# Kernel tuning notes

Measured on AMD Instinct MI355X. Metric: run time of the kernel, lower is better.

The kernel has to match this reference:

```python
import jax, jax.numpy as jnp
import numpy as np

N_NODES = 100000
N_EDGES = 800000
NODE_DIM = 64
EDGE_DIM = 64
GEO_DIM = 8
GEO_OUT = 32
COND_DIM = 512
N_GRAPHS = 64
JOIN_DIM = EDGE_DIM + GEO_OUT  # 96


def setup_inputs() -> dict:
    key = jax.random.key(0)
    ks = jax.random.split(key, 10)
    return {
        "node_feats": jax.random.normal(ks[0], (N_NODES, NODE_DIM), jnp.float32),
        "edge_index": jax.random.randint(ks[1], (2, N_EDGES), 0, N_NODES, jnp.int64),
        "e_geo": jax.random.normal(ks[2], (N_EDGES, GEO_DIM), jnp.float32),
        "cond": jax.random.normal(ks[3], (N_GRAPHS, COND_DIM), jnp.float32),
        "edge_batch_ids": jax.random.randint(ks[4], (N_EDGES,), 0, N_GRAPHS, jnp.int64),
        "Wn": jax.random.normal(ks[5], (NODE_DIM, EDGE_DIM), jnp.float32) / np.sqrt(NODE_DIM),
        "bn": jnp.zeros((EDGE_DIM,), jnp.float32),
        "Wg": jax.random.normal(ks[6], (GEO_DIM, GEO_OUT), jnp.float32) / np.sqrt(GEO_DIM),
        "bg": jnp.zeros((GEO_OUT,), jnp.float32),
        "Wc": jax.random.normal(ks[7], (COND_DIM, 2 * EDGE_DIM), jnp.float32) / np.sqrt(COND_DIM),
        "bc": jnp.zeros((2 * EDGE_DIM,), jnp.float32),
        "Wx": jax.random.normal(ks[8], (JOIN_DIM, EDGE_DIM), jnp.float32) / np.sqrt(JOIN_DIM),
    }


def reference(node_feats, edge_index, e_geo, cond, edge_batch_ids,
              Wn, bn, Wg, bg, Wc, bc, Wx):
    # n_proj: project node features  [N, node_dim] -> [N, edge_dim]
    n_proj = node_feats @ Wn + bn
    # combine_node_attr 'mul': gather to edge endpoints and multiply  [E, edge_dim]
    src = n_proj[edge_index[0]]
    dst = n_proj[edge_index[1]]
    n_join = src * dst
    # e_geo_linear: [E, geo_dim] -> [E, geo_out]
    eg = e_geo @ Wg + bg
    # join features [E, edge_dim + geo_out]
    join = jnp.concatenate([n_join, eg], axis=-1)
    # FilmFusion: cond_proj -> gamma/beta per graph, gather to edges
    gb = cond @ Wc + bc                      # [B, 2*edge_dim]
    gamma, beta = jnp.split(gb, 2, axis=-1)
    gamma = gamma + 1.0
    gamma_e = gamma[edge_batch_ids]          # [E, edge_dim]
    beta_e = beta[edge_batch_ids]
    # x_linear (bias=False), FiLM modulation, relu
    x = join @ Wx
    return jax.nn.relu(x * gamma_e + beta_e)
```

## Files before the change

### kernel.cpp

```cpp
#include <hip/hip_runtime.h>

#define N_NODES   100000
#define N_EDGES   800000
#define NODE_DIM  64
#define EDGE_DIM  64
#define GEO_DIM   8
#define GEO_OUT   32
#define COND_DIM  512
#define N_GRAPHS  64

#define PREP_BLOCKS   65
#define NPROJ_BLOCKS  3125
#define EDGE_BLOCKS   3125

typedef float          f32x4 __attribute__((ext_vector_type(4)));
typedef unsigned       u32x4 __attribute__((ext_vector_type(4)));
typedef unsigned short u16x8 __attribute__((ext_vector_type(8)));
typedef _Float16       f16x8 __attribute__((ext_vector_type(8)));
typedef _Float16       f16x2 __attribute__((ext_vector_type(2)));

__device__ __forceinline__ unsigned short f2h(float f) {
    _Float16 h = (_Float16)f;
    union { _Float16 h; unsigned short u; } cv;
    cv.h = h;
    return cv.u;
}
__device__ __forceinline__ f16x2 cvt2h(float lo, float hi) {
    f16x2 r;
    r[0] = (_Float16)lo;
    r[1] = (_Float16)hi;
    return r;
}

__global__ __launch_bounds__(256) void pre_kernel(
        const float* __restrict__ cond, const float* __restrict__ Wc,
        const float* __restrict__ bc,   const float* __restrict__ Wg,
        const float* __restrict__ bg,   const float* __restrict__ Wx,
        const float* __restrict__ nf,   const float* __restrict__ Wn,
        const float* __restrict__ bn,
        unsigned* __restrict__ gbpack, unsigned short* __restrict__ Bfrag,
        unsigned short* __restrict__ nprojh) {
    int t = threadIdx.x;
    int g = blockIdx.x;
    if (g < N_GRAPHS) {
        __shared__ float condl[COND_DIM];
        __shared__ float gbl[128];
        for (int i = t; i < COND_DIM; i += 256) condl[i] = cond[g * COND_DIM + i];
        __syncthreads();
        if (t < 128) {
            float acc = bc[t];
            #pragma unroll 8
            for (int k = 0; k < COND_DIM; ++k) acc += condl[k] * Wc[k * 128 + t];
            gbl[t] = acc;
        }
        __syncthreads();
        if (t < 64) {
            float gam = gbl[t] + 1.0f;
            float bet = gbl[64 + t];
            float cv = 0.0f;
            #pragma unroll
            for (int i = 0; i < GEO_OUT; ++i) cv += bg[i] * Wx[(64 + i) * 64 + t];
            union { unsigned u; _Float16 h[2]; } pk;
            pk.h[0] = (_Float16)gam;
            pk.h[1] = (_Float16)(bet + cv * gam);
            gbpack[g * 64 + (((t >> 2) ^ (g & 15)) << 2) + (t & 3)] = pk.u;
        }
    } else if (g == N_GRAPHS) {
        for (int idx = t; idx < 6144; idx += 256) {
            int j    = idx & 7;
            int lane = (idx >> 3) & 63;
            int ct   = idx >> 9;
            int c    = ct >> 2, tt = ct & 3;
            int k = c * 32 + ((lane >> 4) & 3) * 8 + j;
            int n = tt * 16 + (lane & 15);
            float val;
            if (k < 64) {
                val = Wx[k * 64 + n];
            } else if (k < 72) {
                float s = 0.f;
                #pragma unroll
                for (int i = 0; i < GEO_OUT; ++i)
                    s += Wg[(k - 64) * GEO_OUT + i] * Wx[(64 + i) * 64 + n];
                val = s;
            } else {
                val = 0.f;
            }
            Bfrag[idx] = f2h(val);
        }
    } else {
        int lane = t & 63;
        int wid    = ((g - PREP_BLOCKS) * 256 + t) >> 6;
        const int nwaves = (NPROJ_BLOCKS * 256) >> 6;
        float wcol[64];
        #pragma unroll
        for (int k = 0; k < 64; ++k) wcol[k] = Wn[k * 64 + lane];
        float bnl = bn[lane];
        for (int node = wid; node < N_NODES; node += 2 * nwaves) {
            int nu0 = __builtin_amdgcn_readfirstlane(node);
            int nu1 = __builtin_amdgcn_readfirstlane(node + nwaves);
            const float* row0 = nf + (size_t)nu0 * 64;
            const float* row1 = nf + (size_t)nu1 * 64;
            float a0 = 0.f, a1 = 0.f, a2 = 0.f, a3 = bnl;
            float c0 = 0.f, c1 = 0.f, c2 = 0.f, c3 = bnl;
            #pragma unroll
            for (int k = 0; k < 64; k += 4) {
                a0 = fmaf(row0[k    ], wcol[k    ], a0);
                a1 = fmaf(row0[k + 1], wcol[k + 1], a1);
                a2 = fmaf(row0[k + 2], wcol[k + 2], a2);
                a3 = fmaf(row0[k + 3], wcol[k + 3], a3);
                c0 = fmaf(row1[k    ], wcol[k    ], c0);
                c1 = fmaf(row1[k + 1], wcol[k + 1], c1);
                c2 = fmaf(row1[k + 2], wcol[k + 2], c2);
                c3 = fmaf(row1[k + 3], wcol[k + 3], c3);
            }
            nprojh[(size_t)nu0 * 64 + lane] = f2h((a0 + a1) + (a2 + a3));
            nprojh[(size_t)nu1 * 64 + lane] = f2h((c0 + c1) + (c2 + c3));
        }
    }
}

__global__ __launch_bounds__(256, 4) void edge_kernel(
        const unsigned short* __restrict__ nprojh,
        const int*   __restrict__ eidx,
        const float* __restrict__ egeo,
        const int*   __restrict__ ebatch,
        const unsigned short* __restrict__ Bfrag,
        const unsigned* __restrict__ gbpack,
        float* __restrict__ out) {
    int lane = threadIdx.x & 63;
    int q  = lane >> 4;
    int mm = lane & 15;
    int wv = threadIdx.x >> 6;

    __shared__ unsigned short Bl[6144];
    __shared__ unsigned GBl[4096];
    __shared__ float ldsT[4][16 * 64];
    float* tileb = ldsT[wv];

    for (int i = threadIdx.x; i < 768; i += 256)
        ((f32x4*)Bl)[i] = ((const f32x4*)Bfrag)[i];
    for (int i = threadIdx.x; i < 4096; i += 256)
        GBl[i] = gbpack[i];
    __syncthreads();

    const int wbase = mm * 64 + q * 4;
    const int rbase = (lane >> 4) * 64 +
                      (((((lane >> 2) & 3) + (lane >> 4)) & 3) << 4) +
                      (lane & 3) * 4;

    int wid = (blockIdx.x * blockDim.x + threadIdx.x) >> 6;
    const int nwaves = (EDGE_BLOCKS * 256) >> 6;
    const int t0 = wid;

    union HU { u16x8 v; f16x2 h[4]; unsigned u[4]; f16x8 f; };

    HU   sA0, sA1, dA0, dA1;  f32x4 gA0 = {0,0,0,0}, gA1 = {0,0,0,0};
    HU   sB0, sB1, dB0, dB1;  f32x4 gB0 = {0,0,0,0}, gB1 = {0,0,0,0};
    int  bqA[4], bqB[4];
    int  siA, diA, bqiA[4];
    int  siB, diB, bqiB[4];

#define LOAD_IDX(sI, dI, bqI, tl)                                              \
    {                                                                          \
        int e0n = (tl) * 16;                                                   \
        sI = __builtin_nontemporal_load(eidx + e0n + mm);                      \
        dI = __builtin_nontemporal_load(eidx + N_EDGES + e0n + mm);            \
        _Pragma("unroll")                                                      \
        for (int c = 0; c < 4; ++c)                                            \
            bqI[c] = __builtin_nontemporal_load(ebatch + e0n + c * 4 + q);     \
    }

#define GATHER(S0, S1, D0, D1, G0, G1, sI, dI, tl)                             \
    {                                                                          \
        const u16x8* ps = (const u16x8*)(nprojh + (size_t)(sI) * 64 + q * 8);  \
        const u16x8* pd = (const u16x8*)(nprojh + (size_t)(dI) * 64 + q * 8);  \
        S0.v = ps[0]; S1.v = ps[4];                                            \
        D0.v = pd[0]; D1.v = pd[4];                                            \
        if (q == 0) {                                                          \
            int e0n = (tl) * 16;                                               \
            G0 = __builtin_nontemporal_load((const f32x4*)(egeo + (size_t)(e0n + mm) * 8));     \
            G1 = __builtin_nontemporal_load((const f32x4*)(egeo + (size_t)(e0n + mm) * 8 + 4)); \
        }                                                                      \
    }

    {
        int si0, di0, si1, di1;
        LOAD_IDX(si0, di0, bqA, t0);
        LOAD_IDX(si1, di1, bqB, t0 + nwaves);
        LOAD_IDX(siA, diA, bqiA, t0 + 2 * nwaves);
        LOAD_IDX(siB, diB, bqiB, t0 + 3 * nwaves);
        GATHER(sA0, sA1, dA0, dA1, gA0, gA1, si0, di0, t0);
        GATHER(sB0, sB1, dB0, dB1, gB0, gB1, si1, di1, t0 + nwaves);
    }

#define BODY(S0, S1, D0, D1, G0, G1, BQ, tl, PREF, sI, dI, bqI)                \
    {                                                                          \
        int e0 = (tl) * 16;                                                    \
        HU A0, A1, A2;                                                         \
        _Pragma("unroll")                                                      \
        for (int j = 0; j < 4; ++j) {                                          \
            A0.h[j] = S0.h[j] * D0.h[j];                     \
            A1.h[j] = S1.h[j] * D1.h[j];                                       \
            A2.u[j] = 0u;                                                      \
        }                                                                      \
        if (q == 0) {                         \
            A2.h[0] = cvt2h(G0[0], G0[1]);                                     \
            A2.h[1] = cvt2h(G0[2], G0[3]);                                     \
            A2.h[2] = cvt2h(G1[0], G1[1]);                                     \
            A2.h[3] = cvt2h(G1[2], G1[3]);                                     \
        }                                                                      \
        if (PREF)                                  \
            GATHER(S0, S1, D0, D1, G0, G1, sI, dI, (tl) + 2 * nwaves);         \
               \
        f32x4 acc[4];                                                          \
        _Pragma("unroll")                                                      \
        for (int t = 0; t < 4; ++t) {                                          \
            f32x4 c = {0.f, 0.f, 0.f, 0.f};                                    \
            c = __builtin_amdgcn_mfma_f32_16x16x32_f16(                        \
                    *(const f16x8*)(Bl + ((0 * 4 + t) * 64 + lane) * 8), A0.f, c, 0, 0, 0); \
            c = __builtin_amdgcn_mfma_f32_16x16x32_f16(                        \
                    *(const f16x8*)(Bl + ((1 * 4 + t) * 64 + lane) * 8), A1.f, c, 0, 0, 0); \
            c = __builtin_amdgcn_mfma_f32_16x16x32_f16(                        \
                    *(const f16x8*)(Bl + ((2 * 4 + t) * 64 + lane) * 8), A2.f, c, 0, 0, 0); \
            acc[t] = c;                                                        \
        }                                                                      \
        \
        _Pragma("unroll")                                                      \
        for (int t = 0; t < 4; ++t)                                            \
            *(f32x4*)&tileb[wbase + (((t + mm) & 3) << 4)] = acc[t];           \
        asm volatile("s_waitcnt lgkmcnt(0)" ::: "memory");      \
        _Pragma("unroll")                                                      \
        for (int c2 = 0; c2 < 4; ++c2) {                                       \
            int b = BQ[c2];                                                    \
            f32x4 v = *(const f32x4*)&tileb[rbase + c2 * 256];                 \
            u32x4 gb = *(const u32x4*)&GBl[b * 64 + ((mm ^ (b & 15)) << 2)];   \
            f32x4 r;                                                           \
            _Pragma("unroll")                                                  \
            for (int i = 0; i < 4; ++i) {                                      \
                union { unsigned u; _Float16 h[2]; } cv;                       \
                cv.u = gb[i];                                                  \
                float x = fmaf(v[i], (float)cv.h[0], (float)cv.h[1]);          \
                r[i] = x > 0.f ? x : 0.f;                                      \
            }                                                                  \
            __builtin_nontemporal_store(r,                                     \
                (f32x4*)(out + (size_t)e0 * 64 + c2 * 256 + lane * 4));        \
        }                                                                      \
        if (PREF) {                                                            \
            _Pragma("unroll")                                                  \
            for (int c2 = 0; c2 < 4; ++c2) BQ[c2] = bqI[c2];                   \
        }                                                                      \
    }

    BODY(sA0, sA1, dA0, dA1, gA0, gA1, bqA, t0,              true,  siA, diA, bqiA);
    BODY(sB0, sB1, dB0, dB1, gB0, gB1, bqB, t0 + nwaves,     true,  siB, diB, bqiB);
    BODY(sA0, sA1, dA0, dA1, gA0, gA1, bqA, t0 + 2 * nwaves, false, siA, diA, bqiA);
    BODY(sB0, sB1, dB0, dB1, gB0, gB1, bqB, t0 + 3 * nwaves, false, siB, diB, bqiB);

#undef BODY
#undef GATHER
#undef LOAD_IDX
}

extern "C" void kernel_launch(void* const* d_in, const int* in_sizes, int n_in,
                              void* d_out, int out_size, void* d_ws, size_t ws_size,
                              hipStream_t stream) {
    const float* node_feats = (const float*)d_in[0];
    const int*   edge_index = (const int*)  d_in[1];
    const float* e_geo      = (const float*)d_in[2];
    const float* cond       = (const float*)d_in[3];
    const int*   ebatch     = (const int*)  d_in[4];
    const float* Wn         = (const float*)d_in[5];
    const float* bn         = (const float*)d_in[6];
    const float* Wg         = (const float*)d_in[7];
    const float* bg         = (const float*)d_in[8];
    const float* Wc         = (const float*)d_in[9];
    const float* bc         = (const float*)d_in[10];
    const float* Wx         = (const float*)d_in[11];
    float* out = (float*)d_out;

    char* ws = (char*)d_ws;
    unsigned*       gbpack = (unsigned*)(ws);
    unsigned short* Bfrag  = (unsigned short*)(ws + 16384);
    unsigned short* nprojh = (unsigned short*)(ws + 32768);

    hipLaunchKernelGGL(pre_kernel, dim3(PREP_BLOCKS + NPROJ_BLOCKS), dim3(256), 0, stream,
                       cond, Wc, bc, Wg, bg, Wx, node_feats, Wn, bn,
                       gbpack, Bfrag, nprojh);
    hipLaunchKernelGGL(edge_kernel, dim3(EDGE_BLOCKS), dim3(256), 0, stream,
                       nprojh, edge_index, e_geo, ebatch, Bfrag, gbpack, out);
}
```

Before: 335.0 us.

## Shrink edge grid and process ten tiles per wave with rolling index prefetch

Cuts the edge kernel grid from 3125 to 1250 blocks. Each wave now handles ten 16-edge tiles instead of four. The fixed-depth index preload is replaced by a rolling pipeline: each body issues the index loads for the tile four steps ahead and the gather for the tile two steps ahead. This spreads the per-block LDS setup (weight fragments and gamma/beta table) over more work and keeps memory requests in flight across iterations. In exchange there is less parallelism at launch, more live registers, and a longer serial chain per wave.

```diff
diff --git a/kernel.cpp b/kernel.cpp
--- a/kernel.cpp
+++ b/kernel.cpp
@@ -11,7 +11,7 @@
 
 #define PREP_BLOCKS   65
 #define NPROJ_BLOCKS  3125
-#define EDGE_BLOCKS   3125
+#define EDGE_BLOCKS   1250
 
 typedef float          f32x4 __attribute__((ext_vector_type(4)));
 typedef unsigned       u32x4 __attribute__((ext_vector_type(4)));
@@ -156,9 +156,9 @@
 
     HU   sA0, sA1, dA0, dA1;  f32x4 gA0 = {0,0,0,0}, gA1 = {0,0,0,0};
     HU   sB0, sB1, dB0, dB1;  f32x4 gB0 = {0,0,0,0}, gB1 = {0,0,0,0};
-    int  bqA[4], bqB[4];
-    int  siA, diA, bqiA[4];
-    int  siB, diB, bqiB[4];
+    int  bqAc[4], bqAn[4], bqBc[4], bqBn[4];
+    int  siA, diA;
+    int  siB, diB;
 
 #define LOAD_IDX(sI, dI, bqI, tl)                                              \
     {                                                                          \
@@ -184,16 +184,15 @@
     }
 
     {
-        int si0, di0, si1, di1;
-        LOAD_IDX(si0, di0, bqA, t0);
-        LOAD_IDX(si1, di1, bqB, t0 + nwaves);
-        LOAD_IDX(siA, diA, bqiA, t0 + 2 * nwaves);
-        LOAD_IDX(siB, diB, bqiB, t0 + 3 * nwaves);
-        GATHER(sA0, sA1, dA0, dA1, gA0, gA1, si0, di0, t0);
-        GATHER(sB0, sB1, dB0, dB1, gB0, gB1, si1, di1, t0 + nwaves);
-    }
-
-#define BODY(S0, S1, D0, D1, G0, G1, BQ, tl, PREF, sI, dI, bqI)                \
+        LOAD_IDX(siA, diA, bqAc, t0);
+        LOAD_IDX(siB, diB, bqBc, t0 + nwaves);
+        GATHER(sA0, sA1, dA0, dA1, gA0, gA1, siA, diA, t0);
+        GATHER(sB0, sB1, dB0, dB1, gB0, gB1, siB, diB, t0 + nwaves);
+        LOAD_IDX(siA, diA, bqAn, t0 + 2 * nwaves);
+        LOAD_IDX(siB, diB, bqBn, t0 + 3 * nwaves);
+    }
+
+#define BODY(S0, S1, D0, D1, G0, G1, BQC, BQN, tl, GEN, IEN, sI, dI)           \
     {                                                                          \
         int e0 = (tl) * 16;                                                    \
         HU A0, A1, A2;                                                         \
@@ -209,7 +208,7 @@
             A2.h[2] = cvt2h(G1[0], G1[1]);                                     \
             A2.h[3] = cvt2h(G1[2], G1[3]);                                     \
         }                                                                      \
-        if (PREF)                                  \
+        if (GEN)                                   \
             GATHER(S0, S1, D0, D1, G0, G1, sI, dI, (tl) + 2 * nwaves);         \
                \
         f32x4 acc[4];                                                          \
@@ -231,7 +230,7 @@
         asm volatile("s_waitcnt lgkmcnt(0)" ::: "memory");      \
         _Pragma("unroll")                                                      \
         for (int c2 = 0; c2 < 4; ++c2) {                                       \
-            int b = BQ[c2];                                                    \
+            int b = BQC[c2];                                                   \
             f32x4 v = *(const f32x4*)&tileb[rbase + c2 * 256];                 \
             u32x4 gb = *(const u32x4*)&GBl[b * 64 + ((mm ^ (b & 15)) << 2)];   \
             f32x4 r;                                                           \
@@ -245,16 +244,24 @@
             __builtin_nontemporal_store(r,                                     \
                 (f32x4*)(out + (size_t)e0 * 64 + c2 * 256 + lane * 4));        \
         }                                                                      \
-        if (PREF) {                                                            \
+        if (GEN) {                               \
             _Pragma("unroll")                                                  \
-            for (int c2 = 0; c2 < 4; ++c2) BQ[c2] = bqI[c2];                   \
-        }                                                                      \
-    }
-
-    BODY(sA0, sA1, dA0, dA1, gA0, gA1, bqA, t0,              true,  siA, diA, bqiA);
-    BODY(sB0, sB1, dB0, dB1, gB0, gB1, bqB, t0 + nwaves,     true,  siB, diB, bqiB);
-    BODY(sA0, sA1, dA0, dA1, gA0, gA1, bqA, t0 + 2 * nwaves, false, siA, diA, bqiA);
-    BODY(sB0, sB1, dB0, dB1, gB0, gB1, bqB, t0 + 3 * nwaves, false, siB, diB, bqiB);
+            for (int c2 = 0; c2 < 4; ++c2) BQC[c2] = BQN[c2];                  \
+        }                                                                      \
+        if (IEN)                                       \
+            LOAD_IDX(sI, dI, BQN, (tl) + 4 * nwaves);                          \
+    }
+
+    BODY(sA0, sA1, dA0, dA1, gA0, gA1, bqAc, bqAn, t0,              true,  true,  siA, diA);
+    BODY(sB0, sB1, dB0, dB1, gB0, gB1, bqBc, bqBn, t0 + 1 * nwaves, true,  true,  siB, diB);
+    BODY(sA0, sA1, dA0, dA1, gA0, gA1, bqAc, bqAn, t0 + 2 * nwaves, true,  true,  siA, diA);
+    BODY(sB0, sB1, dB0, dB1, gB0, gB1, bqBc, bqBn, t0 + 3 * nwaves, true,  true,  siB, diB);
+    BODY(sA0, sA1, dA0, dA1, gA0, gA1, bqAc, bqAn, t0 + 4 * nwaves, true,  true,  siA, diA);
+    BODY(sB0, sB1, dB0, dB1, gB0, gB1, bqBc, bqBn, t0 + 5 * nwaves, true,  true,  siB, diB);
+    BODY(sA0, sA1, dA0, dA1, gA0, gA1, bqAc, bqAn, t0 + 6 * nwaves, true,  false, siA, diA);
+    BODY(sB0, sB1, dB0, dB1, gB0, gB1, bqBc, bqBn, t0 + 7 * nwaves, true,  false, siB, diB);
+    BODY(sA0, sA1, dA0, dA1, gA0, gA1, bqAc, bqAn, t0 + 8 * nwaves, false, false, siA, diA);
+    BODY(sB0, sB1, dB0, dB1, gB0, gB1, bqBc, bqBn, t0 + 9 * nwaves, false, false, siB, diB);
 
 #undef BODY
 #undef GATHER
```

After: 329.5 us. About the same (-1.6%).
